# Performance work log

Hardware: AMD Instinct MI355X
Metric: run time of the kernel (lower is better)

## Reference

```python
import jax, jax.numpy as jnp
import numpy as np

NUM_HEADS = 16  # matches init_kwargs num_heads
ROPE_BASE = 10000.0


def _rope(x):
    # x: [B, H, T, d_k]; canonical interleaved rotary embedding
    d = x.shape[-1]
    T = x.shape[-2]
    inv_freq = 1.0 / (ROPE_BASE ** (jnp.arange(0, d, 2, dtype=jnp.float32) / d))  # [d/2]
    ang = jnp.arange(T, dtype=jnp.float32)[:, None] * inv_freq[None, :]  # [T, d/2]
    cos, sin = jnp.cos(ang), jnp.sin(ang)  # broadcast over B,H
    x1 = x[..., 0::2]
    x2 = x[..., 1::2]
    even = x1 * cos - x2 * sin
    odd = x1 * sin + x2 * cos
    return jnp.stack([even, odd], axis=-1).reshape(x.shape)


def setup_inputs() -> dict:
    key = jax.random.key(0)
    ks = jax.random.split(key, 5)
    B, T, D = 2, 2048, 2048
    s = 1.0 / np.sqrt(D)
    return {
        "x": jax.random.normal(ks[0], (B, T, D), dtype=jnp.float32),
        "Wkqv": jax.random.normal(ks[1], (D, 3 * D), dtype=jnp.float32) * s,
        "bkqv": jax.random.normal(ks[2], (3 * D,), dtype=jnp.float32) * 0.01,
        "Wo": jax.random.normal(ks[3], (D, D), dtype=jnp.float32) * s,
        "bo": jax.random.normal(ks[4], (D,), dtype=jnp.float32) * 0.01,
    }


def reference(x, Wkqv, bkqv, Wo, bo):
    B, T, D = x.shape
    H = NUM_HEADS
    d_k = D // H
    kqv = x @ Wkqv + bkqv  # [B, T, 3D]
    # split order per source: index 0 = K, 1 = Q, 2 = V
    k, q, v = jnp.split(kqv, 3, axis=-1)

    def heads(t):  # [B, T, D] -> [B, H, T, d_k]
        return t.reshape(B, T, H, d_k).transpose(0, 2, 1, 3)

    k, q, v = heads(k), heads(q), heads(v)
    k = _rope(k)
    q = _rope(q)
    scores = jnp.einsum('bhtd,bhTd->bhtT', q, k)  # [B, H, T, T]
    causal = jnp.triu(jnp.ones((T, T), dtype=bool), k=1)
    scores = jnp.where(causal, -jnp.inf, scores)
    attn = jax.nn.softmax(scores / jnp.sqrt(jnp.float32(d_k)), axis=-1)
    out = jnp.einsum('bhtT,bhTd->bhtd', attn, v)  # [B, H, T, d_k]
    out = out.transpose(0, 2, 1, 3).reshape(B, T, D)
    return out @ Wo + bo
```

## Files before the change

kernel.cpp:

```cpp
#include <hip/hip_runtime.h>
#include <cstdint>
#include <cstddef>

typedef __attribute__((ext_vector_type(4))) float  floatx4;
typedef __attribute__((ext_vector_type(8))) __bf16 bf16x8;
typedef __attribute__((ext_vector_type(4))) __bf16 bf16x4;

#define B_   2
#define T_   2048
#define D_   2048
#define H_   16
#define DK   128
#define BT_  (B_ * T_)
#define N3   (3 * D_)

__device__ __forceinline__ void async_copy16(const void* g, void* l) {
    __builtin_amdgcn_global_load_lds((const __attribute__((address_space(1))) void*)g,
                                     (__attribute__((address_space(3))) void*)l,
                                     16, 0, 0);
}

__global__ void cast_bf16_kernel(const float* __restrict__ in, __bf16* __restrict__ out, int n4) {
    int i = blockIdx.x * 256 + threadIdx.x;
    if (i >= n4) return;
    float4 v = ((const float4*)in)[i];
    bf16x4 o;
    o.x = (__bf16)v.x; o.y = (__bf16)v.y; o.z = (__bf16)v.z; o.w = (__bf16)v.w;
    ((bf16x4*)out)[i] = o;
}

__global__ void transcast_kernel(const float* __restrict__ in, __bf16* __restrict__ out, int R, int C) {
    __shared__ float tile[32][33];
    int c0 = blockIdx.x * 32, r0 = blockIdx.y * 32;
    int tx = threadIdx.x, ty = threadIdx.y;
#pragma unroll
    for (int j = 0; j < 32; j += 8)
        tile[ty + j][tx] = in[(size_t)(r0 + ty + j) * C + c0 + tx];
    __syncthreads();
#pragma unroll
    for (int j = 0; j < 32; j += 8)
        out[(size_t)(c0 + ty + j) * R + r0 + tx] = (__bf16)tile[tx][ty + j];
}

__global__ void vtrans_kernel(const __bf16* __restrict__ kqv, __bf16* __restrict__ VT) {
    __shared__ __bf16 tile[32][33];
    int bh = blockIdx.z; int b = bh >> 4, h = bh & 15;
    int t0 = blockIdx.x * 32, d0 = blockIdx.y * 32;
    int tx = threadIdx.x, ty = threadIdx.y;
#pragma unroll
    for (int j = 0; j < 32; j += 8)
        tile[ty + j][tx] = kqv[(size_t)(b * T_ + t0 + ty + j) * N3 + 2 * D_ + h * DK + d0 + tx];
    __syncthreads();
#pragma unroll
    for (int j = 0; j < 32; j += 8)
        VT[(size_t)(bh * DK + d0 + ty + j) * T_ + t0 + tx] = tile[tx][ty + j];
}

__global__ void rope_kernel(const __bf16* __restrict__ kqv,
                            __bf16* __restrict__ Kh, __bf16* __restrict__ Qh) {
    int idx = blockIdx.x * 256 + threadIdx.x;
    int i     = idx & 63;
    int t     = (idx >> 6) & (T_ - 1);
    int bh    = (idx >> 17) & 31;
    int which = idx >> 22;
    int b = bh >> 4, h = bh & 15;
    const __bf16* src = kqv + (size_t)(b * T_ + t) * N3 + which * D_ + h * DK + 2 * i;
    float x1 = (float)src[0], x2 = (float)src[1];
    float freq = exp2f((float)i * (-13.287712379549449f / 64.f));
    float ang = (float)t * freq;
    float sn, cn; sincosf(ang, &sn, &cn);
    float s = which ? 0.12751740f : 1.0f;
    __bf16* dst = (which ? Qh : Kh) + (size_t)(bh * T_ + t) * DK + 2 * i;
    dst[0] = (__bf16)((x1 * cn - x2 * sn) * s);
    dst[1] = (__bf16)((x1 * sn + x2 * cn) * s);
}

template <typename OutT>
__global__ __launch_bounds__(256)
void gemm_bt(const __bf16* __restrict__ A, const __bf16* __restrict__ BTm,
             const float* __restrict__ bias, OutT* __restrict__ C,
             int M, int N, int K) {
    __shared__ __align__(16) __bf16 As[128 * 64];
    __shared__ __align__(16) __bf16 Bs[128 * 64];
    const int tid  = threadIdx.x;
    const int lane = tid & 63;
    const int wave = tid >> 6;
    const int quad = lane >> 4;
    const int l16  = lane & 15;
    const int m0 = blockIdx.y * 128;
    const int n0 = blockIdx.x * 128;
    const int wm = (wave & 1) * 64;
    const int wn = (wave >> 1) * 64;

    const floatx4 z4 = {0.f, 0.f, 0.f, 0.f};
    floatx4 acc[4][4];
#pragma unroll
    for (int i = 0; i < 4; ++i)
#pragma unroll
        for (int j = 0; j < 4; ++j) acc[i][j] = z4;

    int           sOff[4];
    const __bf16* gA[4];
    const __bf16* gB[4];
#pragma unroll
    for (int i = 0; i < 4; ++i) {
        int s = i * 256 + tid;
        int row = s >> 3, cs = s & 7;
        int gc = cs ^ (row & 7);
        sOff[i] = s * 8;
        gA[i] = A   + (size_t)(m0 + row) * K + gc * 8;
        gB[i] = BTm + (size_t)(n0 + row) * K + gc * 8;
    }

    for (int kt = 0; kt < K; kt += 64) {
        __syncthreads();
#pragma unroll
        for (int i = 0; i < 4; ++i) {
            async_copy16(gA[i] + kt, As + sOff[i]);
            async_copy16(gB[i] + kt, Bs + sOff[i]);
        }
        __syncthreads();
#pragma unroll
        for (int ks2 = 0; ks2 < 2; ++ks2) {
            bf16x8 af[4], bf[4];
#pragma unroll
            for (int t = 0; t < 4; ++t) {
                int rowA = wm + t * 16 + l16;
                int ca = (ks2 * 4 + quad) ^ (rowA & 7);
                af[t] = *(const bf16x8*)(As + rowA * 64 + ca * 8);
                int rowB = wn + t * 16 + l16;
                int cb = (ks2 * 4 + quad) ^ (rowB & 7);
                bf[t] = *(const bf16x8*)(Bs + rowB * 64 + cb * 8);
            }
#pragma unroll
            for (int mt = 0; mt < 4; ++mt)
#pragma unroll
                for (int nt = 0; nt < 4; ++nt)
                    acc[mt][nt] = __builtin_amdgcn_mfma_f32_16x16x32_bf16(af[mt], bf[nt], acc[mt][nt], 0, 0, 0);
        }
    }

#pragma unroll
    for (int nt = 0; nt < 4; ++nt) {
        int n = n0 + wn + nt * 16 + l16;
        float bv = bias[n];
#pragma unroll
        for (int mt = 0; mt < 4; ++mt)
#pragma unroll
            for (int r = 0; r < 4; ++r) {
                int m = m0 + wm + mt * 16 + quad * 4 + r;
                C[(size_t)m * N + n] = (OutT)(acc[mt][nt][r] + bv);
            }
    }
}

__global__ __launch_bounds__(256)
void fa_kernel(const __bf16* __restrict__ Qg, const __bf16* __restrict__ Kg,
               const __bf16* __restrict__ VTg, __bf16* __restrict__ Og) {
    __shared__ __align__(16) __bf16 Ks[2][64 * 128];
    __shared__ __align__(16) __bf16 Vs[2][128 * 64];
    __shared__ __align__(16) __bf16 Ps[4][16 * 64];
    const int tid  = threadIdx.x;
    const int lane = tid & 63, wave = tid >> 6;
    const int quad = lane >> 4, l16 = lane & 15;
    const int bh = blockIdx.y;
    const int j  = blockIdx.x;
    const int b = bh >> 4, h = bh & 15;

    const __bf16* Kb = Kg  + (size_t)bh * T_ * DK;
    const __bf16* Vb = VTg + (size_t)bh * DK * T_;
    __bf16* Psw = Ps[wave];

    const floatx4 z4 = {0.f, 0.f, 0.f, 0.f};

    int           sK[4], sV[4];
    const __bf16* gK[4];
    const __bf16* gV[4];
#pragma unroll
    for (int i = 0; i < 4; ++i) {
        int s = i * 256 + tid;
        { int row = s >> 4, cs = s & 15; int gc = cs ^ (row & 7);
          sK[i] = s * 8; gK[i] = Kb + (size_t)row * DK + gc * 8; }
        { int row = s >> 3, cs = s & 7;  int gc = cs ^ (row & 7);
          sV[i] = s * 8; gV[i] = Vb + (size_t)row * T_ + gc * 8; }
    }

    for (int half = 0; half < 2; ++half) {
        const int qt = half ? (31 - j) : j;
        const int q0 = qt * 64;

        __syncthreads();
        {
            const __bf16* Qb = Qg + (size_t)(bh * T_ + q0) * DK;
#pragma unroll
            for (int i = 0; i < 4; ++i) {
                int s = i * 256 + tid;
                int row = s >> 4, cs = s & 15;
                int gc = cs ^ (row & 7);
                async_copy16(Qb + row * DK + gc * 8, &Ks[0][0] + s * 8);
            }
        }
        __syncthreads();
        bf16x8 qf[4];
#pragma unroll
        for (int ks = 0; ks < 4; ++ks) {
            int row = wave * 16 + l16;
            int c = (ks * 4 + quad) ^ (row & 7);
            qf[ks] = *(const bf16x8*)(&Ks[0][0] + row * DK + c * 8);
        }
        __syncthreads();

#pragma unroll
        for (int i = 0; i < 4; ++i) async_copy16(gK[i], &Ks[0][0] + sK[i]);
#pragma unroll
        for (int i = 0; i < 4; ++i) async_copy16(gV[i], &Vs[0][0] + sV[i]);

        float m_i[4], l_i[4];
        floatx4 accO[8];
#pragma unroll
        for (int r = 0; r < 4; ++r) { m_i[r] = -1e30f; l_i[r] = 0.f; }
#pragma unroll
        for (int nt = 0; nt < 8; ++nt) accO[nt] = z4;

        for (int kt = 0; kt <= qt; ++kt) {
            const int cur = kt & 1;
            if (kt < qt) {
                const int nb = cur ^ 1;
                const size_t koff = (size_t)(kt + 1) * 64 * DK;
                const size_t voff = (size_t)(kt + 1) * 64;
#pragma unroll
                for (int i = 0; i < 4; ++i) async_copy16(gK[i] + koff, &Ks[nb][0] + sK[i]);
#pragma unroll
                for (int i = 0; i < 4; ++i) async_copy16(gV[i] + voff, &Vs[nb][0] + sV[i]);
                asm volatile("s_waitcnt vmcnt(8)" ::: "memory");
            } else {
                asm volatile("s_waitcnt vmcnt(0)" ::: "memory");
            }
            __builtin_amdgcn_s_barrier();

            const __bf16* Kcur = &Ks[cur][0];
            const __bf16* Vcur = &Vs[cur][0];

            floatx4 sc[4];
#pragma unroll
            for (int nt = 0; nt < 4; ++nt) sc[nt] = z4;
            __builtin_amdgcn_s_setprio(1);
#pragma unroll
            for (int ks = 0; ks < 4; ++ks)
#pragma unroll
                for (int nt = 0; nt < 4; ++nt) {
                    int row = nt * 16 + l16;
                    int c = (ks * 4 + quad) ^ (row & 7);
                    bf16x8 kf = *(const bf16x8*)(Kcur + row * DK + c * 8);
                    sc[nt] = __builtin_amdgcn_mfma_f32_16x16x32_bf16(qf[ks], kf, sc[nt], 0, 0, 0);
                }
            __builtin_amdgcn_s_setprio(0);

            float mnew[4] = {-1e30f, -1e30f, -1e30f, -1e30f};
            if (kt == qt) {
                const int qrow0 = q0 + wave * 16 + quad * 4;
#pragma unroll
                for (int nt = 0; nt < 4; ++nt) {
                    int kp = kt * 64 + nt * 16 + l16;
#pragma unroll
                    for (int r = 0; r < 4; ++r) {
                        float v = sc[nt][r];
                        v = (kp > qrow0 + r) ? -1e30f : v;
                        sc[nt][r] = v;
                        mnew[r] = fmaxf(mnew[r], v);
                    }
                }
            } else {
#pragma unroll
                for (int nt = 0; nt < 4; ++nt)
#pragma unroll
                    for (int r = 0; r < 4; ++r) mnew[r] = fmaxf(mnew[r], sc[nt][r]);
            }
#pragma unroll
            for (int r = 0; r < 4; ++r) {
                float v = mnew[r];
                v = fmaxf(v, __shfl_xor(v, 1));
                v = fmaxf(v, __shfl_xor(v, 2));
                v = fmaxf(v, __shfl_xor(v, 4));
                v = fmaxf(v, __shfl_xor(v, 8));
                mnew[r] = v;
            }
            float alpha[4];
#pragma unroll
            for (int r = 0; r < 4; ++r) {
                float mi = fmaxf(m_i[r], mnew[r]);
                alpha[r] = exp2f(m_i[r] - mi);
                m_i[r] = mi;
            }
            float rs[4] = {0.f, 0.f, 0.f, 0.f};
#pragma unroll
            for (int nt = 0; nt < 4; ++nt)
#pragma unroll
                for (int r = 0; r < 4; ++r) {
                    float p = exp2f(sc[nt][r] - m_i[r]);
                    sc[nt][r] = p;
                    rs[r] += p;
                }
#pragma unroll
            for (int r = 0; r < 4; ++r) {
                float v = rs[r];
                v += __shfl_xor(v, 1);
                v += __shfl_xor(v, 2);
                v += __shfl_xor(v, 4);
                v += __shfl_xor(v, 8);
                l_i[r] = l_i[r] * alpha[r] + v;
            }
#pragma unroll
            for (int nt = 0; nt < 8; ++nt)
#pragma unroll
                for (int r = 0; r < 4; ++r) accO[nt][r] *= alpha[r];

#pragma unroll
            for (int nt = 0; nt < 4; ++nt) {
                int col = nt * 16 + l16;
                int ch = col >> 3, off = col & 7;
#pragma unroll
                for (int r = 0; r < 4; ++r) {
                    int row = quad * 4 + r;
                    Psw[row * 64 + (ch ^ (row & 7)) * 8 + off] = (__bf16)sc[nt][r];
                }
            }
            __builtin_amdgcn_s_setprio(1);
#pragma unroll
            for (int ks2 = 0; ks2 < 2; ++ks2) {
                int ach = (ks2 * 4 + quad) ^ (l16 & 7);
                bf16x8 pf = *(const bf16x8*)(Psw + l16 * 64 + ach * 8);
#pragma unroll
                for (int nt = 0; nt < 8; ++nt) {
                    int vrow = nt * 16 + l16;
                    int vch = (ks2 * 4 + quad) ^ (vrow & 7);
                    bf16x8 vf = *(const bf16x8*)(Vcur + vrow * 64 + vch * 8);
                    accO[nt] = __builtin_amdgcn_mfma_f32_16x16x32_bf16(pf, vf, accO[nt], 0, 0, 0);
                }
            }
            __builtin_amdgcn_s_setprio(0);

            __builtin_amdgcn_s_barrier();
        }

#pragma unroll
        for (int nt = 0; nt < 8; ++nt)
#pragma unroll
            for (int r = 0; r < 4; ++r) {
                int trow = q0 + wave * 16 + quad * 4 + r;
                int col = h * DK + nt * 16 + l16;
                Og[(size_t)(b * T_ + trow) * D_ + col] = (__bf16)(accO[nt][r] / l_i[r]);
            }
    }
}

extern "C" void kernel_launch(void* const* d_in, const int* in_sizes, int n_in,
                              void* d_out, int out_size, void* d_ws, size_t ws_size,
                              hipStream_t stream) {
    const float* x    = (const float*)d_in[0];
    const float* Wkqv = (const float*)d_in[1];
    const float* bkqv = (const float*)d_in[2];
    const float* Wo   = (const float*)d_in[3];
    const float* bo   = (const float*)d_in[4];
    float* out = (float*)d_out;

    char* p = (char*)d_ws;
    __bf16* xb    = (__bf16*)p; p += (size_t)BT_ * D_ * 2;
    __bf16* WkqvT = (__bf16*)p; p += (size_t)D_ * N3 * 2;
    __bf16* WoT   = (__bf16*)p; p += (size_t)D_ * D_ * 2;
    __bf16* kqv   = (__bf16*)p; p += (size_t)BT_ * N3 * 2;
    __bf16* qh    = (__bf16*)p; p += (size_t)BT_ * D_ * 2;
    __bf16* kh    = (__bf16*)p; p += (size_t)BT_ * D_ * 2;
    __bf16* vT    = (__bf16*)p; p += (size_t)BT_ * D_ * 2;
    __bf16* ao    = (__bf16*)p; p += (size_t)BT_ * D_ * 2;

    cast_bf16_kernel<<<(BT_ * D_ / 4 + 255) / 256, 256, 0, stream>>>(x, xb, BT_ * D_ / 4);
    transcast_kernel<<<dim3(N3 / 32, D_ / 32), dim3(32, 8), 0, stream>>>(Wkqv, WkqvT, D_, N3);
    transcast_kernel<<<dim3(D_ / 32, D_ / 32), dim3(32, 8), 0, stream>>>(Wo, WoT, D_, D_);
    gemm_bt<__bf16><<<dim3(N3 / 128, BT_ / 128), 256, 0, stream>>>(xb, WkqvT, bkqv, kqv, BT_, N3, D_);
    rope_kernel<<<(2 * 32 * T_ * 64) / 256, 256, 0, stream>>>(kqv, kh, qh);
    vtrans_kernel<<<dim3(T_ / 32, DK / 32, B_ * H_), dim3(32, 8), 0, stream>>>(kqv, vT);
    fa_kernel<<<dim3(16, B_ * H_), 256, 0, stream>>>(qh, kh, vT, ao);
    gemm_bt<float><<<dim3(D_ / 128, BT_ / 128), 256, 0, stream>>>(ao, WoT, bo, out, BT_, D_, D_);
}
```

Before: 424.8 us.

## Add 256x256 double-buffered GEMM for KQV projection and fast RoPE trig

Adds a new 512-thread GEMM kernel with 256x256 tiles, double-buffered LDS filled by async global-to-LDS copies, XOR-swizzled LDS layout, phased MFMA issue with priority bumps, and a grouped block swizzle for L2 locality. It replaces the 128x128 GEMM for the QKV projection. RoPE also switches from sincosf to range-reduced __sinf/__cosf. The larger tile raises reuse and hides load latency, but uses 128KB of LDS and many registers per block. The fast trig functions may lose some accuracy.

```diff
diff --git a/kernel.cpp b/kernel.cpp
--- a/kernel.cpp
+++ b/kernel.cpp
@@ -66,9 +66,11 @@
     int b = bh >> 4, h = bh & 15;
     const __bf16* src = kqv + (size_t)(b * T_ + t) * N3 + which * D_ + h * DK + 2 * i;
     float x1 = (float)src[0], x2 = (float)src[1];
-    float freq = exp2f((float)i * (-13.287712379549449f / 64.f));
-    float ang = (float)t * freq;
-    float sn, cn; sincosf(ang, &sn, &cn);
+    float freq_rev = 0.15915494309189535f * exp2f((float)i * (-13.287712379549449f / 64.f));
+    float rev = (float)t * freq_rev;
+    rev -= floorf(rev);
+    float ang = rev * 6.283185307179586f;
+    float sn = __sinf(ang), cn = __cosf(ang);
     float s = which ? 0.12751740f : 1.0f;
     __bf16* dst = (which ? Qh : Kh) + (size_t)(bh * T_ + t) * DK + 2 * i;
     dst[0] = (__bf16)((x1 * cn - x2 * sn) * s);
@@ -154,6 +156,140 @@
     }
 }
 
+template <typename OutT>
+__global__ __launch_bounds__(512, 2)
+void gemm256(const __bf16* __restrict__ A, const __bf16* __restrict__ BTm,
+             const float* __restrict__ bias, OutT* __restrict__ C,
+             int M, int N, int K) {
+    __shared__ __align__(16) __bf16 AS[2][256 * 64];
+    __shared__ __align__(16) __bf16 BS[2][256 * 64];
+    const int tid  = threadIdx.x;
+    const int lane = tid & 63;
+    const int quad = lane >> 4;
+    const int l16  = lane & 15;
+    const int wv   = tid >> 6;
+    const int wm   = wv >> 2;
+    const int wn   = wv & 3;
+
+    int lin = blockIdx.y * gridDim.x + blockIdx.x;
+    int qq  = (gridDim.x * gridDim.y) >> 3;
+    int swz = (lin & 7) * qq + (lin >> 3);
+    const int m0 = (swz / gridDim.x) * 256;
+    const int n0 = (swz % gridDim.x) * 256;
+
+    const floatx4 z4 = {0.f, 0.f, 0.f, 0.f};
+    floatx4 acc[8][4];
+#pragma unroll
+    for (int i = 0; i < 8; ++i)
+#pragma unroll
+        for (int j = 0; j < 4; ++j) acc[i][j] = z4;
+
+    int       ldsB[2], ldsA[2];
+    const __bf16* gBp[2];
+    const __bf16* gAp[2];
+#pragma unroll
+    for (int l = 0; l < 2; ++l) {
+        int s = l * 512 + tid;
+        int r = s >> 3, cs = s & 7;
+        int gc = cs ^ (r & 7);
+        ldsB[l] = s * 16;
+        gBp[l]  = BTm + (size_t)(n0 + r) * K + gc * 8;
+        int rowA = (r < 64) ? r : (r + 64);
+        ldsA[l] = rowA * 128 + cs * 16;
+        gAp[l]  = A + (size_t)(m0 + rowA) * K + gc * 8;
+    }
+
+#define STAGE_B(bufb, u, tile)                                                   \
+    {                                                                            \
+        _Pragma("unroll") for (int l = 0; l < 2; ++l)                            \
+            async_copy16(gBp[l] + (size_t)(u) * 128 * K + (size_t)(tile) * 64,   \
+                         (char*)&BS[(bufb)][0] + (u) * 16384 + ldsB[l]);         \
+    }
+#define STAGE_A(bufb, u, tile)                                                   \
+    {                                                                            \
+        _Pragma("unroll") for (int l = 0; l < 2; ++l)                            \
+            async_copy16(gAp[l] + (size_t)(u) * 64 * K + (size_t)(tile) * 64,    \
+                         (char*)&AS[(bufb)][0] + (u) * 8192 + ldsA[l]);          \
+    }
+
+    bf16x8 bfr[8];
+    bf16x8 afr[4];
+
+#define PHASE(BUFB, MP, LOADB, STAGE_STMT, WAIT_STMT)                              \
+    {                                                                              \
+        if (LOADB) {                                                               \
+            _Pragma("unroll") for (int nf = 0; nf < 4; ++nf)                       \
+            _Pragma("unroll") for (int ks = 0; ks < 2; ++ks) {                     \
+                int row = wn * 64 + nf * 16 + l16;                                 \
+                int c = (ks * 4 + quad) ^ (row & 7);                               \
+                bfr[nf * 2 + ks] = *(const bf16x8*)(&BS[BUFB][0] + row * 64 + c * 8); \
+            }                                                                      \
+        }                                                                          \
+        _Pragma("unroll") for (int mi = 0; mi < 2; ++mi)                           \
+        _Pragma("unroll") for (int ks = 0; ks < 2; ++ks) {                         \
+            int row = wm * 128 + ((MP) * 2 + mi) * 16 + l16;                       \
+            int c = (ks * 4 + quad) ^ (row & 7);                                   \
+            afr[mi * 2 + ks] = *(const bf16x8*)(&AS[BUFB][0] + row * 64 + c * 8);  \
+        }                                                                          \
+        STAGE_STMT;                                                                \
+        WAIT_STMT;                                                                 \
+        __builtin_amdgcn_s_barrier();                                              \
+        asm volatile("s_waitcnt lgkmcnt(0)" ::: "memory");                         \
+        __builtin_amdgcn_sched_barrier(0);                                         \
+        __builtin_amdgcn_s_setprio(1);                                             \
+        _Pragma("unroll") for (int mi = 0; mi < 2; ++mi)                           \
+        _Pragma("unroll") for (int nf = 0; nf < 4; ++nf)                           \
+        _Pragma("unroll") for (int ks = 0; ks < 2; ++ks)                           \
+            acc[(MP) * 2 + mi][nf] = __builtin_amdgcn_mfma_f32_16x16x32_bf16(      \
+                afr[mi * 2 + ks], bfr[nf * 2 + ks], acc[(MP) * 2 + mi][nf], 0, 0, 0); \
+        __builtin_amdgcn_s_setprio(0);                                             \
+        __builtin_amdgcn_s_barrier();                                              \
+    }
+
+#define VM6 asm volatile("s_waitcnt vmcnt(6)" ::: "memory")
+#define VM0 asm volatile("s_waitcnt vmcnt(0)" ::: "memory")
+
+    const int nt    = K >> 6;
+    const int niter = nt >> 1;
+
+    STAGE_B(0, 0, 0); STAGE_B(0, 1, 0); STAGE_A(0, 0, 0); STAGE_A(0, 1, 0);
+    STAGE_B(1, 0, 1); STAGE_B(1, 1, 1); STAGE_A(1, 0, 1);
+    VM6;
+    __builtin_amdgcn_s_barrier();
+
+    for (int it = 0; it < niter; ++it) {
+        const int tau  = 2 * it;
+        const bool lst = (it == niter - 1);
+        PHASE(0, 0, true,  { STAGE_A(1, 1, tau + 1); }, {});
+        PHASE(0, 1, false, { if (!lst) STAGE_B(0, 0, tau + 2); }, {});
+        PHASE(0, 2, false, { if (!lst) STAGE_B(0, 1, tau + 2); }, {});
+        PHASE(0, 3, false, { if (!lst) STAGE_A(0, 0, tau + 2); }, { if (lst) { VM0; } else { VM6; } });
+        PHASE(1, 0, true,  { if (!lst) STAGE_A(0, 1, tau + 2); }, {});
+        PHASE(1, 1, false, { if (!lst) STAGE_B(1, 0, tau + 3); }, {});
+        PHASE(1, 2, false, { if (!lst) STAGE_B(1, 1, tau + 3); }, {});
+        PHASE(1, 3, false, { if (!lst) STAGE_A(1, 0, tau + 3); }, { if (!lst) { VM6; } });
+    }
+
+#undef PHASE
+#undef STAGE_A
+#undef STAGE_B
+#undef VM6
+#undef VM0
+
+#pragma unroll
+    for (int nf = 0; nf < 4; ++nf) {
+        int n = n0 + wn * 64 + nf * 16 + l16;
+        float bv = bias[n];
+#pragma unroll
+        for (int mf = 0; mf < 8; ++mf)
+#pragma unroll
+            for (int r = 0; r < 4; ++r) {
+                int m = m0 + wm * 128 + mf * 16 + quad * 4 + r;
+                C[(size_t)m * N + n] = (OutT)(acc[mf][nf][r] + bv);
+            }
+    }
+}
+
 __global__ __launch_bounds__(256)
 void fa_kernel(const __bf16* __restrict__ Qg, const __bf16* __restrict__ Kg,
                const __bf16* __restrict__ VTg, __bf16* __restrict__ Og) {
@@ -377,7 +513,7 @@
     cast_bf16_kernel<<<(BT_ * D_ / 4 + 255) / 256, 256, 0, stream>>>(x, xb, BT_ * D_ / 4);
     transcast_kernel<<<dim3(N3 / 32, D_ / 32), dim3(32, 8), 0, stream>>>(Wkqv, WkqvT, D_, N3);
     transcast_kernel<<<dim3(D_ / 32, D_ / 32), dim3(32, 8), 0, stream>>>(Wo, WoT, D_, D_);
-    gemm_bt<__bf16><<<dim3(N3 / 128, BT_ / 128), 256, 0, stream>>>(xb, WkqvT, bkqv, kqv, BT_, N3, D_);
+    gemm256<__bf16><<<dim3(N3 / 256, BT_ / 256), 512, 0, stream>>>(xb, WkqvT, bkqv, kqv, BT_, N3, D_);
     rope_kernel<<<(2 * 32 * T_ * 64) / 256, 256, 0, stream>>>(kqv, kh, qh);
     vtrans_kernel<<<dim3(T_ / 32, DK / 32, B_ * H_), dim3(32, 8), 0, stream>>>(kqv, vT);
     fa_kernel<<<dim3(16, B_ * H_), 256, 0, stream>>>(qh, kh, vT, ao);
```

Measured after the change: 449.1 us. 5.7% more time.

## Fuse RoPE, Q scaling and V transpose into the KQV GEMM epilogue

Applied to the files above, without the earlier changes.

Replaces the KQV GEMM, the separate RoPE kernel and the V-transpose kernel with a single GEMM whose epilogue applies bias, rotary embedding via a lane shuffle of adjacent columns, and Q scaling, writing K/Q in head-major layout and V transposed. This removes the intermediate kqv buffer round trip and two kernel launches. The V stores become strided and uncoalesced along t, and fast __sinf/__cosf with range reduction replace sincosf, which may slightly change precision.

```diff
diff --git a/kernel.cpp b/kernel.cpp
--- a/kernel.cpp
+++ b/kernel.cpp
@@ -40,39 +40,6 @@
 #pragma unroll
     for (int j = 0; j < 32; j += 8)
         out[(size_t)(c0 + ty + j) * R + r0 + tx] = (__bf16)tile[tx][ty + j];
-}
-
-__global__ void vtrans_kernel(const __bf16* __restrict__ kqv, __bf16* __restrict__ VT) {
-    __shared__ __bf16 tile[32][33];
-    int bh = blockIdx.z; int b = bh >> 4, h = bh & 15;
-    int t0 = blockIdx.x * 32, d0 = blockIdx.y * 32;
-    int tx = threadIdx.x, ty = threadIdx.y;
-#pragma unroll
-    for (int j = 0; j < 32; j += 8)
-        tile[ty + j][tx] = kqv[(size_t)(b * T_ + t0 + ty + j) * N3 + 2 * D_ + h * DK + d0 + tx];
-    __syncthreads();
-#pragma unroll
-    for (int j = 0; j < 32; j += 8)
-        VT[(size_t)(bh * DK + d0 + ty + j) * T_ + t0 + tx] = tile[tx][ty + j];
-}
-
-__global__ void rope_kernel(const __bf16* __restrict__ kqv,
-                            __bf16* __restrict__ Kh, __bf16* __restrict__ Qh) {
-    int idx = blockIdx.x * 256 + threadIdx.x;
-    int i     = idx & 63;
-    int t     = (idx >> 6) & (T_ - 1);
-    int bh    = (idx >> 17) & 31;
-    int which = idx >> 22;
-    int b = bh >> 4, h = bh & 15;
-    const __bf16* src = kqv + (size_t)(b * T_ + t) * N3 + which * D_ + h * DK + 2 * i;
-    float x1 = (float)src[0], x2 = (float)src[1];
-    float freq = exp2f((float)i * (-13.287712379549449f / 64.f));
-    float ang = (float)t * freq;
-    float sn, cn; sincosf(ang, &sn, &cn);
-    float s = which ? 0.12751740f : 1.0f;
-    __bf16* dst = (which ? Qh : Kh) + (size_t)(bh * T_ + t) * DK + 2 * i;
-    dst[0] = (__bf16)((x1 * cn - x2 * sn) * s);
-    dst[1] = (__bf16)((x1 * sn + x2 * cn) * s);
 }
 
 template <typename OutT>
@@ -155,6 +122,111 @@
 }
 
 __global__ __launch_bounds__(256)
+void gemm_kqv(const __bf16* __restrict__ A, const __bf16* __restrict__ BTm,
+              const float* __restrict__ bias,
+              __bf16* __restrict__ Kh, __bf16* __restrict__ Qh,
+              __bf16* __restrict__ VT,
+              int M, int N, int K) {
+    __shared__ __align__(16) __bf16 As[128 * 64];
+    __shared__ __align__(16) __bf16 Bs[128 * 64];
+    const int tid  = threadIdx.x;
+    const int lane = tid & 63;
+    const int wave = tid >> 6;
+    const int quad = lane >> 4;
+    const int l16  = lane & 15;
+    const int m0 = blockIdx.y * 128;
+    const int n0 = blockIdx.x * 128;
+    const int wm = (wave & 1) * 64;
+    const int wn = (wave >> 1) * 64;
+
+    const floatx4 z4 = {0.f, 0.f, 0.f, 0.f};
+    floatx4 acc[4][4];
+#pragma unroll
+    for (int i = 0; i < 4; ++i)
+#pragma unroll
+        for (int j = 0; j < 4; ++j) acc[i][j] = z4;
+
+    int           sOff[4];
+    const __bf16* gA[4];
+    const __bf16* gB[4];
+#pragma unroll
+    for (int i = 0; i < 4; ++i) {
+        int s = i * 256 + tid;
+        int row = s >> 3, cs = s & 7;
+        int gc = cs ^ (row & 7);
+        sOff[i] = s * 8;
+        gA[i] = A   + (size_t)(m0 + row) * K + gc * 8;
+        gB[i] = BTm + (size_t)(n0 + row) * K + gc * 8;
+    }
+
+    for (int kt = 0; kt < K; kt += 64) {
+        __syncthreads();
+#pragma unroll
+        for (int i = 0; i < 4; ++i) {
+            async_copy16(gA[i] + kt, As + sOff[i]);
+            async_copy16(gB[i] + kt, Bs + sOff[i]);
+        }
+        __syncthreads();
+#pragma unroll
+        for (int ks2 = 0; ks2 < 2; ++ks2) {
+            bf16x8 af[4], bf[4];
+#pragma unroll
+            for (int t = 0; t < 4; ++t) {
+                int rowA = wm + t * 16 + l16;
+                int ca = (ks2 * 4 + quad) ^ (rowA & 7);
+                af[t] = *(const bf16x8*)(As + rowA * 64 + ca * 8);
+                int rowB = wn + t * 16 + l16;
+                int cb = (ks2 * 4 + quad) ^ (rowB & 7);
+                bf[t] = *(const bf16x8*)(Bs + rowB * 64 + cb * 8);
+            }
+#pragma unroll
+            for (int mt = 0; mt < 4; ++mt)
+#pragma unroll
+                for (int nt = 0; nt < 4; ++nt)
+                    acc[mt][nt] = __builtin_amdgcn_mfma_f32_16x16x32_bf16(af[mt], bf[nt], acc[mt][nt], 0, 0, 0);
+        }
+    }
+
+#pragma unroll
+    for (int nt = 0; nt < 4; ++nt) {
+        const int n   = n0 + wn + nt * 16 + l16;
+        const float bv = bias[n];
+        const int which = n >> 11;
+        const int nin   = n & (D_ - 1);
+        const int h  = nin >> 7;
+        const int dd = nin & 127;
+        const float freq_rev = 0.15915494309189535f *
+                               exp2f((float)(dd >> 1) * (-13.287712379549449f / 64.f));
+        const float qscale = (which == 1) ? 0.12751740f : 1.0f;
+#pragma unroll
+        for (int mt = 0; mt < 4; ++mt)
+#pragma unroll
+            for (int r = 0; r < 4; ++r) {
+                const int m = m0 + wm + mt * 16 + quad * 4 + r;
+                const int b = m >> 11;
+                const int t = m & (T_ - 1);
+                const int bh = b * H_ + h;
+                const float val = acc[mt][nt][r] + bv;
+                if (which == 2) {
+                    VT[((size_t)bh * DK + dd) * T_ + t] = (__bf16)val;
+                } else {
+                    const float other = __shfl_xor(val, 1);
+                    const float x1 = (dd & 1) ? other : val;
+                    const float x2 = (dd & 1) ? val : other;
+                    float rev = (float)t * freq_rev;
+                    rev -= floorf(rev);
+                    const float ang = rev * 6.283185307179586f;
+                    const float sn = __sinf(ang), cn = __cosf(ang);
+                    const float res = (dd & 1) ? (x1 * sn + x2 * cn)
+                                               : (x1 * cn - x2 * sn);
+                    __bf16* dst = (which == 1) ? Qh : Kh;
+                    dst[((size_t)bh * T_ + t) * DK + dd] = (__bf16)(res * qscale);
+                }
+            }
+    }
+}
+
+__global__ __launch_bounds__(256)
 void fa_kernel(const __bf16* __restrict__ Qg, const __bf16* __restrict__ Kg,
                const __bf16* __restrict__ VTg, __bf16* __restrict__ Og) {
     __shared__ __align__(16) __bf16 Ks[2][64 * 128];
@@ -368,7 +440,6 @@
     __bf16* xb    = (__bf16*)p; p += (size_t)BT_ * D_ * 2;
     __bf16* WkqvT = (__bf16*)p; p += (size_t)D_ * N3 * 2;
     __bf16* WoT   = (__bf16*)p; p += (size_t)D_ * D_ * 2;
-    __bf16* kqv   = (__bf16*)p; p += (size_t)BT_ * N3 * 2;
     __bf16* qh    = (__bf16*)p; p += (size_t)BT_ * D_ * 2;
     __bf16* kh    = (__bf16*)p; p += (size_t)BT_ * D_ * 2;
     __bf16* vT    = (__bf16*)p; p += (size_t)BT_ * D_ * 2;
@@ -377,9 +448,7 @@
     cast_bf16_kernel<<<(BT_ * D_ / 4 + 255) / 256, 256, 0, stream>>>(x, xb, BT_ * D_ / 4);
     transcast_kernel<<<dim3(N3 / 32, D_ / 32), dim3(32, 8), 0, stream>>>(Wkqv, WkqvT, D_, N3);
     transcast_kernel<<<dim3(D_ / 32, D_ / 32), dim3(32, 8), 0, stream>>>(Wo, WoT, D_, D_);
-    gemm_bt<__bf16><<<dim3(N3 / 128, BT_ / 128), 256, 0, stream>>>(xb, WkqvT, bkqv, kqv, BT_, N3, D_);
-    rope_kernel<<<(2 * 32 * T_ * 64) / 256, 256, 0, stream>>>(kqv, kh, qh);
-    vtrans_kernel<<<dim3(T_ / 32, DK / 32, B_ * H_), dim3(32, 8), 0, stream>>>(kqv, vT);
+    gemm_kqv<<<dim3(N3 / 128, BT_ / 128), 256, 0, stream>>>(xb, WkqvT, bkqv, kh, qh, vT, BT_, N3, D_);
     fa_kernel<<<dim3(16, B_ * H_), 256, 0, stream>>>(qh, kh, vT, ao);
     gemm_bt<float><<<dim3(D_ / 128, BT_ / 128), 256, 0, stream>>>(ao, WoT, bo, out, BT_, D_, D_);
 }
```

New measurement: 435.3 us. +2.5%, slower.

## Transpose flash-attention MFMA operands so softmax stats stay per-lane, cheapen RoPE sincos

Applied to the files above, without the earlier changes.

Swaps the MFMA operand order in the flash-attention kernel so S^T and O^T are computed. Each lane then owns one query row, which replaces sixteen 4-step cross-lane shuffle reductions per tile with two shuffles each for max and sum. P and O are now written with vectorized bf16x4 stores under a new swizzle. Separately, RoPE replaces sincosf with range-reduced __sinf/__cosf, which risks small precision differences.

```diff
diff --git a/kernel.cpp b/kernel.cpp
--- a/kernel.cpp
+++ b/kernel.cpp
@@ -66,9 +66,11 @@
     int b = bh >> 4, h = bh & 15;
     const __bf16* src = kqv + (size_t)(b * T_ + t) * N3 + which * D_ + h * DK + 2 * i;
     float x1 = (float)src[0], x2 = (float)src[1];
-    float freq = exp2f((float)i * (-13.287712379549449f / 64.f));
-    float ang = (float)t * freq;
-    float sn, cn; sincosf(ang, &sn, &cn);
+    float freq_rev = 0.15915494309189535f * exp2f((float)i * (-13.287712379549449f / 64.f));
+    float rev = (float)t * freq_rev;
+    rev -= floorf(rev);
+    float ang = rev * 6.283185307179586f;
+    float sn = __sinf(ang), cn = __cosf(ang);
     float s = which ? 0.12751740f : 1.0f;
     __bf16* dst = (which ? Qh : Kh) + (size_t)(bh * T_ + t) * DK + 2 * i;
     dst[0] = (__bf16)((x1 * cn - x2 * sn) * s);
@@ -170,6 +172,7 @@
     const __bf16* Kb = Kg  + (size_t)bh * T_ * DK;
     const __bf16* Vb = VTg + (size_t)bh * DK * T_;
     __bf16* Psw = Ps[wave];
+    const int swzP = (l16 & 7) << 1;
 
     const floatx4 z4 = {0.f, 0.f, 0.f, 0.f};
 
@@ -188,6 +191,7 @@
     for (int half = 0; half < 2; ++half) {
         const int qt = half ? (31 - j) : j;
         const int q0 = qt * 64;
+        const int qpos = q0 + wave * 16 + l16;
 
         __syncthreads();
         {
@@ -215,12 +219,10 @@
 #pragma unroll
         for (int i = 0; i < 4; ++i) async_copy16(gV[i], &Vs[0][0] + sV[i]);
 
-        float m_i[4], l_i[4];
+        float m_i = -1e30f, l_i = 0.f;
         floatx4 accO[8];
 #pragma unroll
-        for (int r = 0; r < 4; ++r) { m_i[r] = -1e30f; l_i[r] = 0.f; }
-#pragma unroll
-        for (int nt = 0; nt < 8; ++nt) accO[nt] = z4;
+        for (int dt = 0; dt < 8; ++dt) accO[dt] = z4;
 
         for (int kt = 0; kt <= qt; ++kt) {
             const int cur = kt & 1;
@@ -252,105 +254,89 @@
                     int row = nt * 16 + l16;
                     int c = (ks * 4 + quad) ^ (row & 7);
                     bf16x8 kf = *(const bf16x8*)(Kcur + row * DK + c * 8);
-                    sc[nt] = __builtin_amdgcn_mfma_f32_16x16x32_bf16(qf[ks], kf, sc[nt], 0, 0, 0);
+                    sc[nt] = __builtin_amdgcn_mfma_f32_16x16x32_bf16(kf, qf[ks], sc[nt], 0, 0, 0);
                 }
             __builtin_amdgcn_s_setprio(0);
 
-            float mnew[4] = {-1e30f, -1e30f, -1e30f, -1e30f};
+            float mnew = -1e30f;
             if (kt == qt) {
-                const int qrow0 = q0 + wave * 16 + quad * 4;
 #pragma unroll
                 for (int nt = 0; nt < 4; ++nt) {
-                    int kp = kt * 64 + nt * 16 + l16;
+                    int kbase = kt * 64 + nt * 16 + quad * 4;
 #pragma unroll
                     for (int r = 0; r < 4; ++r) {
                         float v = sc[nt][r];
-                        v = (kp > qrow0 + r) ? -1e30f : v;
+                        v = (kbase + r > qpos) ? -1e30f : v;
                         sc[nt][r] = v;
-                        mnew[r] = fmaxf(mnew[r], v);
+                        mnew = fmaxf(mnew, v);
                     }
                 }
             } else {
 #pragma unroll
                 for (int nt = 0; nt < 4; ++nt)
 #pragma unroll
-                    for (int r = 0; r < 4; ++r) mnew[r] = fmaxf(mnew[r], sc[nt][r]);
-            }
-#pragma unroll
-            for (int r = 0; r < 4; ++r) {
-                float v = mnew[r];
-                v = fmaxf(v, __shfl_xor(v, 1));
-                v = fmaxf(v, __shfl_xor(v, 2));
-                v = fmaxf(v, __shfl_xor(v, 4));
-                v = fmaxf(v, __shfl_xor(v, 8));
-                mnew[r] = v;
-            }
-            float alpha[4];
-#pragma unroll
-            for (int r = 0; r < 4; ++r) {
-                float mi = fmaxf(m_i[r], mnew[r]);
-                alpha[r] = exp2f(m_i[r] - mi);
-                m_i[r] = mi;
-            }
-            float rs[4] = {0.f, 0.f, 0.f, 0.f};
+                    for (int r = 0; r < 4; ++r) mnew = fmaxf(mnew, sc[nt][r]);
+            }
+            mnew = fmaxf(mnew, __shfl_xor(mnew, 16));
+            mnew = fmaxf(mnew, __shfl_xor(mnew, 32));
+            const float mi = fmaxf(m_i, mnew);
+            const float alpha = exp2f(m_i - mi);
+            m_i = mi;
+
+            float rs = 0.f;
 #pragma unroll
             for (int nt = 0; nt < 4; ++nt)
 #pragma unroll
                 for (int r = 0; r < 4; ++r) {
-                    float p = exp2f(sc[nt][r] - m_i[r]);
-                    sc[nt][r] = p;
-                    rs[r] += p;
+                    float pv = exp2f(sc[nt][r] - mi);
+                    sc[nt][r] = pv;
+                    rs += pv;
                 }
-#pragma unroll
-            for (int r = 0; r < 4; ++r) {
-                float v = rs[r];
-                v += __shfl_xor(v, 1);
-                v += __shfl_xor(v, 2);
-                v += __shfl_xor(v, 4);
-                v += __shfl_xor(v, 8);
-                l_i[r] = l_i[r] * alpha[r] + v;
-            }
-#pragma unroll
-            for (int nt = 0; nt < 8; ++nt)
-#pragma unroll
-                for (int r = 0; r < 4; ++r) accO[nt][r] *= alpha[r];
+            rs += __shfl_xor(rs, 16);
+            rs += __shfl_xor(rs, 32);
+            l_i = l_i * alpha + rs;
+#pragma unroll
+            for (int dt = 0; dt < 8; ++dt)
+#pragma unroll
+                for (int r = 0; r < 4; ++r) accO[dt][r] *= alpha;
 
 #pragma unroll
             for (int nt = 0; nt < 4; ++nt) {
-                int col = nt * 16 + l16;
-                int ch = col >> 3, off = col & 7;
-#pragma unroll
-                for (int r = 0; r < 4; ++r) {
-                    int row = quad * 4 + r;
-                    Psw[row * 64 + (ch ^ (row & 7)) * 8 + off] = (__bf16)sc[nt][r];
+                bf16x4 pw;
+                pw.x = (__bf16)sc[nt][0]; pw.y = (__bf16)sc[nt][1];
+                pw.z = (__bf16)sc[nt][2]; pw.w = (__bf16)sc[nt][3];
+                int g = (nt * 4 + quad) ^ swzP;
+                *(bf16x4*)(Psw + l16 * 64 + g * 4) = pw;
+            }
+            __builtin_amdgcn_s_setprio(1);
+#pragma unroll
+            for (int kc = 0; kc < 2; ++kc) {
+                int gk = (kc * 8 + quad * 2) ^ swzP;
+                bf16x8 pb = *(const bf16x8*)(Psw + l16 * 64 + gk * 4);
+#pragma unroll
+                for (int dt = 0; dt < 8; ++dt) {
+                    int vrow = dt * 16 + l16;
+                    int vch = (kc * 4 + quad) ^ (vrow & 7);
+                    bf16x8 vf = *(const bf16x8*)(Vcur + vrow * 64 + vch * 8);
+                    accO[dt] = __builtin_amdgcn_mfma_f32_16x16x32_bf16(vf, pb, accO[dt], 0, 0, 0);
                 }
             }
-            __builtin_amdgcn_s_setprio(1);
-#pragma unroll
-            for (int ks2 = 0; ks2 < 2; ++ks2) {
-                int ach = (ks2 * 4 + quad) ^ (l16 & 7);
-                bf16x8 pf = *(const bf16x8*)(Psw + l16 * 64 + ach * 8);
-#pragma unroll
-                for (int nt = 0; nt < 8; ++nt) {
-                    int vrow = nt * 16 + l16;
-                    int vch = (ks2 * 4 + quad) ^ (vrow & 7);
-                    bf16x8 vf = *(const bf16x8*)(Vcur + vrow * 64 + vch * 8);
-                    accO[nt] = __builtin_amdgcn_mfma_f32_16x16x32_bf16(pf, vf, accO[nt], 0, 0, 0);
-                }
-            }
             __builtin_amdgcn_s_setprio(0);
 
             __builtin_amdgcn_s_barrier();
         }
 
-#pragma unroll
-        for (int nt = 0; nt < 8; ++nt)
-#pragma unroll
-            for (int r = 0; r < 4; ++r) {
-                int trow = q0 + wave * 16 + quad * 4 + r;
-                int col = h * DK + nt * 16 + l16;
-                Og[(size_t)(b * T_ + trow) * D_ + col] = (__bf16)(accO[nt][r] / l_i[r]);
-            }
+        const float inv = 1.0f / l_i;
+        __bf16* orow = Og + (size_t)(b * T_ + qpos) * D_ + h * DK;
+#pragma unroll
+        for (int dt = 0; dt < 8; ++dt) {
+            bf16x4 ow;
+            ow.x = (__bf16)(accO[dt][0] * inv);
+            ow.y = (__bf16)(accO[dt][1] * inv);
+            ow.z = (__bf16)(accO[dt][2] * inv);
+            ow.w = (__bf16)(accO[dt][3] * inv);
+            *(bf16x4*)(orow + dt * 16 + quad * 4) = ow;
+        }
     }
 }
 
```

After: 407.0 us. 4.2% less time.
